# Kernel optimization log

Measured on AMD Instinct MI355X. Metric: run time of the kernel, lower is better.

Reference implementation:

```python
import jax, jax.numpy as jnp
import numpy as np

NUM_CLASSES = 7
CLASS_WEIGHT = 1.0
BOX_WEIGHT = 1.0


def _linear_sum_assignment(cost):
    """Exact Hungarian via shortest augmenting paths (Jonker-Volgenant style).
    Matches scipy.optimize.linear_sum_assignment for rectangular matrices:
    returns (row_ind, col_ind) of length min(n, m), row_ind sorted ascending."""
    C = np.asarray(cost, dtype=np.float64)
    transposed = C.shape[0] > C.shape[1]
    if transposed:
        C = C.T
    n, m = C.shape  # n <= m
    u = np.zeros(n + 1)
    v = np.zeros(m + 1)
    p = np.zeros(m + 1, dtype=np.int64)    # p[j]: row matched to col j (1-based); 0 = free
    way = np.zeros(m + 1, dtype=np.int64)
    for i in range(1, n + 1):
        p[0] = i
        j0 = 0
        minv = np.full(m + 1, np.inf)
        used = np.zeros(m + 1, dtype=bool)
        while True:
            used[j0] = True
            i0 = p[j0]
            cur = C[i0 - 1] - u[i0] - v[1:]
            free = ~used[1:]
            better = free & (cur < minv[1:])
            minv[1:][better] = cur[better]
            way[1:][better] = j0
            masked = np.where(free, minv[1:], np.inf)
            j0n = int(np.argmin(masked)) + 1
            delta = masked[j0n - 1]
            uj = np.nonzero(used)[0]
            u[p[uj]] += delta
            v[uj] -= delta
            minv[1:][free] -= delta
            j0 = j0n
            if p[j0] == 0:
                break
        while j0 != 0:   # augment along alternating path
            j1 = way[j0]
            p[j0] = p[j1]
            j0 = j1
    cols = np.nonzero(p[1:] > 0)[0]
    rows = p[1:][cols] - 1
    if transposed:
        rows, cols = cols, rows
    order = np.argsort(rows)
    return rows[order], cols[order]


def _cost_matrices(pred_logits, pred_boxes, gt_labels, gt_boxes):
    """Batched cost: class_weight * (-log_softmax gathered at gt labels) + box_weight * L1 cdist on xyz."""
    B, Q, _ = pred_logits.shape
    M = gt_labels.shape[1]
    log_probs = jax.nn.log_softmax(pred_logits, axis=-1)                       # (B,Q,C)
    idx = jnp.broadcast_to(gt_labels[:, None, :], (B, Q, M))
    class_cost = -jnp.take_along_axis(log_probs, idx, axis=2)                  # (B,Q,M)
    box_cost = jnp.sum(jnp.abs(pred_boxes[:, :, None, :3] - gt_boxes[:, None, :, :3]), axis=-1)  # (B,Q,M)
    return CLASS_WEIGHT * class_cost + BOX_WEIGHT * box_cost


def _matched_loss(pred_logits, pred_boxes, gt_labels, gt_boxes, rows, cols):
    B = pred_logits.shape[0]
    bidx = jnp.arange(B)[:, None]
    ml = pred_logits[bidx, rows]          # (B,M,C) matched logits
    mb = pred_boxes[bidx, rows]           # (B,M,7) matched boxes
    gl = gt_labels[bidx, cols]            # (B,M)
    gb = gt_boxes[bidx, cols]             # (B,M,7)
    logp = jax.nn.log_softmax(ml, axis=-1)
    ce = -jnp.mean(jnp.take_along_axis(logp, gl[..., None], axis=-1)[..., 0], axis=1)  # (B,)
    l1 = jnp.mean(jnp.abs(mb - gb), axis=(1, 2))                                       # (B,)
    return jnp.mean(CLASS_WEIGHT * ce + BOX_WEIGHT * l1)


def setup_inputs() -> dict:
    key = jax.random.key(0)
    k1, k2, k3, k4 = jax.random.split(key, 4)
    B, Q, M = 128, 900, 100
    return {
        'pred_logits': jax.random.normal(k1, (B, Q, NUM_CLASSES), dtype=jnp.float32),
        'pred_boxes': jax.random.normal(k2, (B, Q, 7), dtype=jnp.float32),
        'gt_labels': jax.random.randint(k3, (B, M), 0, NUM_CLASSES, dtype=jnp.int32),
        'gt_boxes': jax.random.normal(k4, (B, M, 7), dtype=jnp.float32),
    }


def reference(pred_logits, pred_boxes, gt_labels, gt_boxes):
    B = pred_logits.shape[0]
    M = gt_labels.shape[1]
    # Assignment is done on detached costs (host-side), matching the original module.
    cost = np.asarray(_cost_matrices(pred_logits, pred_boxes, gt_labels, gt_boxes))
    rows = np.zeros((B, M), dtype=np.int64)
    cols = np.zeros((B, M), dtype=np.int64)
    for b in range(B):
        r, c = _linear_sum_assignment(cost[b])
        rows[b], cols[b] = r, c
    return _matched_loss(pred_logits, pred_boxes, gt_labels, gt_boxes,
                         jnp.asarray(rows), jnp.asarray(cols))
```

## Files before the change

kernel.cpp:

```cpp
#include <hip/hip_runtime.h>
#include <math.h>


#define NQ   900
#define NG   100
#define NC   7
#define CPL  15
#define ROUNDS 12
#define INFF __builtin_inff()

__device__ __forceinline__ float readlane_f(float x, int l) {
  return __int_as_float(__builtin_amdgcn_readlane(__float_as_int(x), l));
}
template<int CTRL>
__device__ __forceinline__ float dpp_min_step(float x) {
  int y = __builtin_amdgcn_update_dpp(__float_as_int(x), __float_as_int(x),
                                      CTRL, 0xf, 0xf, false);
  return fminf(x, __int_as_float(y));
}
__device__ __forceinline__ float wave_min_b(float x) {
  x = dpp_min_step<0x111>(x);
  x = dpp_min_step<0x112>(x);
  x = dpp_min_step<0x114>(x);
  x = dpp_min_step<0x118>(x);
  x = dpp_min_step<0x142>(x);
  x = dpp_min_step<0x143>(x);
  return __int_as_float(__builtin_amdgcn_readlane(__float_as_int(x), 63));
}
template<int CTRL>
__device__ __forceinline__ float dpp_add_step(float x) {
  int y = __builtin_amdgcn_update_dpp(0, __float_as_int(x),
                                      CTRL, 0xf, 0xf, true);
  return x + __int_as_float(y);
}
__device__ __forceinline__ float wave_sum_b(float x) {
  x = dpp_add_step<0x111>(x);
  x = dpp_add_step<0x112>(x);
  x = dpp_add_step<0x114>(x);
  x = dpp_add_step<0x118>(x);
  x = dpp_add_step<0x142>(x);
  x = dpp_add_step<0x143>(x);
  return __int_as_float(__builtin_amdgcn_readlane(__float_as_int(x), 63));
}
__device__ __forceinline__ void gl_lds16(const float* g, float* lds_base) {
  __builtin_amdgcn_global_load_lds(
      (const __attribute__((address_space(1))) unsigned int*)g,
      (__attribute__((address_space(3))) unsigned int*)lds_base, 16, 0, 0);
}
__device__ __forceinline__ float sel7v(float a0,float a1,float a2,float a3,
                                       float a4,float a5,float a6,int lab){
  float r = a0;
  r = lab==1 ? a1 : r;  r = lab==2 ? a2 : r;  r = lab==3 ? a3 : r;
  r = lab==4 ? a4 : r;  r = lab==5 ? a5 : r;  r = lab==6 ? a6 : r;
  return r;
}

__global__ __launch_bounds__(256, 1) void hungarian_fused_kernel(
    const float* __restrict__ logits, const float* __restrict__ pboxes,
    const int* __restrict__ glabels, const float* __restrict__ gboxes,
    float* __restrict__ out, float inv_B)
{
  const int b = blockIdx.x, tid = threadIdx.x;
  const int lane = tid & 63, w = tid >> 6;

  __shared__ __align__(16) float s_raw[NQ * NC];
  __shared__ __align__(16) float s_nlpT[NC * 1024];
  __shared__ __align__(16) float s_pb[960 * NC];
  __shared__ __align__(16) float s_gb[NG * NC];
  __shared__ __align__(16) int   s_glab[NG];
  __shared__ float s_u[NG + 1];
  __shared__ float s_v[CPL * 64];
  __shared__ int   s_p[NQ];
  __shared__ unsigned s_bid[NQ];
  __shared__ int   s_rmatch[NG];
  __shared__ float s_bm1[NG], s_bm2[NG];
  __shared__ int   s_bc[NG];
  __shared__ int   s_freelist[NG];
  __shared__ int   s_nfree;
  __shared__ float s_f1v[NG]; __shared__ int s_f1c[NG];
  __shared__ float s_f2v[NG]; __shared__ int s_f2c[NG];
  __shared__ int   s_mlist[128];

  {
    const float* Lg = logits + (size_t)b * NQ * NC;
    const float* Pg = pboxes + (size_t)b * NQ * NC;
    const float* Gg = gboxes + (size_t)b * NG * NC;
    const int*   Bg = glabels + (size_t)b * NG;
    #pragma unroll
    for (int t = 0; t < 7; t++) {
      int i = (t << 8) + tid;
      if (i < (NQ * NC) / 4) {
        gl_lds16(Lg + i * 4, s_raw + ((t << 8) + (w << 6)) * 4);
        gl_lds16(Pg + i * 4, s_pb  + ((t << 8) + (w << 6)) * 4);
      }
    }
    if (tid < (NG * NC) / 4) gl_lds16(Gg + tid * 4, s_gb + (w << 6) * 4);
    if (tid < NG / 4) gl_lds16((const float*)Bg + tid * 4, (float*)s_glab);
    for (int i = tid; i < (960 - NQ) * NC; i += 256) s_pb[NQ * NC + i] = 0.f;
    for (int c = tid; c < NQ; c += 256) { s_p[c] = 0x7fffffff; s_bid[c] = 0xFFFFFFFFu; }
    for (int i = tid; i < CPL * 64; i += 256) s_v[i] = 0.f;
    if (tid == 0) s_u[0] = 0.f;
  }
  __syncthreads();

  for (int i = tid; i < 960; i += 256) {
    int L = i & 63, t = i >> 6;
    int q = L * CPL + t;
    float o[NC];
    if (q < NQ) {
      float x[NC];
      #pragma unroll
      for (int c = 0; c < NC; c++) x[c] = s_raw[q * NC + c];
      float mx = x[0];
      #pragma unroll
      for (int c = 1; c < NC; c++) mx = fmaxf(mx, x[c]);
      float tt[NC]; float se = 0.f;
      #pragma unroll
      for (int c = 0; c < NC; c++) { tt[c] = x[c] - mx; se += __expf(tt[c]); }
      float lg = __logf(se);
      #pragma unroll
      for (int c = 0; c < NC; c++) o[c] = lg - tt[c];
    } else {
      #pragma unroll
      for (int c = 0; c < NC; c++) o[c] = INFF;
    }
    #pragma unroll
    for (int c = 0; c < NC; c++) s_nlpT[c * 1024 + t * 64 + L] = o[c];
  }
  __syncthreads();

  const bool lval = (lane < NQ / CPL);
  float cpx[CPL], cpy[CPL], cpz[CPL];
  #pragma unroll
  for (int t = 0; t < CPL; t++) {
    int c = lane * CPL + t;
    cpx[t]=s_pb[c*NC+0]; cpy[t]=s_pb[c*NC+1]; cpz[t]=s_pb[c*NC+2];
  }

  for (int rl = 0; rl < 25; rl++) {
    int r = w * 25 + rl;
    int lab = s_glab[r];
    float gx = s_gb[r*NC+0], gy = s_gb[r*NC+1], gz = s_gb[r*NC+2];
    float m1 = INFF; int c1t = 0;
    #pragma unroll
    for (int t = 0; t < CPL; t++) {
      float nl = s_nlpT[lab*1024 + t*64 + lane];
      float bs = fabsf(cpx[t]-gx)+fabsf(cpy[t]-gy)+fabsf(cpz[t]-gz);
      float cost = nl + bs;
      bool lt1 = cost < m1;
      c1t = lt1 ? t : c1t;
      m1 = fminf(m1, cost);
    }
    float w1 = wave_min_b(m1);
    unsigned long long mk = __ballot(m1 == w1);
    int src = (int)__builtin_ctzll(mk);
    int col = __builtin_amdgcn_readlane(lane * CPL + c1t, src);
    if (lane == 0) {
      s_u[r + 1] = w1;
      s_bc[r] = col;
      atomicMin(&s_p[col], r + 1);
    }
  }
  __syncthreads();
  for (int c = tid; c < NQ; c += 256) if (s_p[c] == 0x7fffffff) s_p[c] = 0;
  if (tid < NG) {
    int c = s_bc[tid];
    s_rmatch[tid] = (s_p[c] == tid + 1) ? c + 1 : 0;
  }
  __syncthreads();

  for (int round = 0; round < ROUNDS; round++) {
    if (tid == 0) s_nfree = 0;
    __syncthreads();
    if (tid < NG && s_rmatch[tid] == 0) {
      int ix = atomicAdd(&s_nfree, 1);
      s_freelist[ix] = tid;
    }
    __syncthreads();
    int nf = s_nfree;
    if (nf == 0) break;
    for (int fi = w; fi < nf; fi += 4) {
      int r = s_freelist[fi];
      int lab = s_glab[r];
      float gx = s_gb[r*NC+0], gy = s_gb[r*NC+1], gz = s_gb[r*NC+2];
      float m1 = INFF, m2 = INFF; int c1t = 0;
      #pragma unroll
      for (int t = 0; t < CPL; t++) {
        float nl = s_nlpT[lab*1024 + t*64 + lane];
        float vv = s_v[t*64 + lane];
        float bs = fabsf(cpx[t]-gx)+fabsf(cpy[t]-gy)+fabsf(cpz[t]-gz);
        float cost = (nl + bs) - vv;
        bool lt1 = cost < m1;
        m2 = lt1 ? m1 : fminf(m2, cost);
        c1t = lt1 ? t : c1t;
        m1 = fminf(m1, cost);
      }
      float w1 = wave_min_b(m1);
      unsigned long long mk = __ballot(m1 == w1);
      int src = (int)__builtin_ctzll(mk);
      int col1 = __builtin_amdgcn_readlane(lane * CPL + c1t, src);
      float alt = (lane == src) ? m2 : m1;
      float w2 = wave_min_b(alt);
      if (lane == 0) {
        s_bm1[r] = w1; s_bm2[r] = w2; s_bc[r] = col1;
        atomicMin(&s_bid[col1],
                  (__float_as_uint(w1) & 0xFFFFFF80u) | (unsigned)(r + 1));
      }
    }
    __syncthreads();
    for (int fi = tid; fi < nf; fi += 256) {
      int r = s_freelist[fi];
      int c = s_bc[r];
      if ((s_bid[c] & 0x7Fu) == (unsigned)(r + 1)) {
        int dold = s_p[c];
        s_p[c] = r + 1;
        s_rmatch[r] = c + 1;
        if (dold > 0) s_rmatch[dold - 1] = 0;
        s_u[r + 1] = s_bm2[r];
        s_v[(c % CPL) * 64 + (c / CPL)] -= (s_bm2[r] - s_bm1[r]);
      }
    }
    __syncthreads();
    for (int fi = tid; fi < nf; fi += 256)
      s_bid[s_bc[s_freelist[fi]]] = 0xFFFFFFFFu;
    __syncthreads();
  }

  unsigned fmask = 0;
  if (lval) {
    #pragma unroll
    for (int t = 0; t < CPL; t++)
      if (s_p[lane * CPL + t] == 0) fmask |= (1u << t);
  }

  auto top2row = [&](int lab, float gx, float gy, float gz,
                     float &o1v, int &o1c, float &o2v, int &o2c) {
    float m1 = INFF, m2 = INFF; int c1 = 0, c2 = 0;
    #pragma unroll
    for (int t = 0; t < CPL; t++) {
      float nl = s_nlpT[lab*1024 + t*64 + lane];
      float bs = fabsf(cpx[t]-gx)+fabsf(cpy[t]-gy)+fabsf(cpz[t]-gz);
      float cost = nl + bs;
      cost = ((fmask >> t) & 1u) ? cost : INFF;
      bool lt1 = cost < m1;
      bool lt2 = cost < m2;
      c2 = lt1 ? c1 : (lt2 ? t : c2);
      m2 = lt1 ? m1 : fminf(m2, cost);
      c1 = lt1 ? t : c1;
      m1 = fminf(m1, cost);
    }
    float w1 = wave_min_b(m1);
    unsigned long long mk = __ballot(m1 == w1);
    int src = (int)__builtin_ctzll(mk);
    int col1 = __builtin_amdgcn_readlane(lane * CPL + c1, src);
    float alt = (lane == src) ? m2 : m1;
    int  altc = (lane == src) ? c2 : c1;
    float w2 = wave_min_b(alt);
    unsigned long long mk2 = __ballot(alt == w2);
    int src2 = (int)__builtin_ctzll(mk2);
    int col2 = __builtin_amdgcn_readlane(lane * CPL + altc, src2);
    o1v = w1; o1c = col1; o2v = w2; o2c = col2;
  };

  for (int rl = 0; rl < 25; rl++) {
    int r = w * 25 + rl;
    int lab = s_glab[r];
    float gx = s_gb[r*NC+0], gy = s_gb[r*NC+1], gz = s_gb[r*NC+2];
    float v1, v2; int cc1, cc2;
    top2row(lab, gx, gy, gz, v1, cc1, v2, cc2);
    if (lane == 0) {
      s_f1v[r] = v1; s_f1c[r] = cc1; s_f2v[r] = v2; s_f2c[r] = cc2;
    }
  }
  __syncthreads();
  if (w != 0) return;

  volatile float* vu = s_u;

  const bool r1ok = (lane < NG - 64);
  int   rlab0 = s_glab[lane];
  float rgx0 = s_gb[lane*NC+0], rgy0 = s_gb[lane*NC+1], rgz0 = s_gb[lane*NC+2];
  int   rlab1 = 0; float rgx1=0.f, rgy1=0.f, rgz1=0.f;
  if (r1ok) {
    int r = 64 + lane;
    rlab1 = s_glab[r];
    rgx1 = s_gb[r*NC+0]; rgy1 = s_gb[r*NC+1]; rgz1 = s_gb[r*NC+2];
  }
  float ru0 = vu[lane + 1];
  float ru1 = r1ok ? vu[lane + 65] : 0.f;
  float rf1v0 = s_f1v[lane];       int rf1c0 = s_f1c[lane];
  float rf2v0 = s_f2v[lane];       int rf2c0 = s_f2c[lane];
  float rf1v1 = r1ok ? s_f1v[64+lane] : INFF; int rf1c1 = r1ok ? s_f1c[64+lane] : -1;
  float rf2v1 = r1ok ? s_f2v[64+lane] : INFF; int rf2c1 = r1ok ? s_f2c[64+lane] : -1;

  bool lose0 = (s_rmatch[lane] == 0);
  bool lose1 = r1ok && (s_rmatch[64 + lane] == 0);
  unsigned long long fm0 = __ballot(lose0);
  unsigned long long fm1 = __ballot(lose1);

  int NM = 0;
  #pragma unroll
  for (int t = 0; t < CPL; t++) {
    int c = lane * CPL + t;
    bool has = lval && (s_p[c] > 0);
    unsigned long long m = __ballot(has);
    int pos = NM + (int)__popcll(m & ((1ull << lane) - 1ull));
    if (has) s_mlist[pos] = c;
    NM += (int)__popcll(m);
  }

  int   mcol[2]  = {-1,-1};
  int   mprow[2] = {0,0};
  float mpu[2]   = {0.f,0.f};
  float mv[2]    = {0.f,0.f};
  float mx[2]={0,0}, my[2]={0,0}, mz[2]={0,0};
  float mn0[2],mn1[2],mn2[2],mn3[2],mn4[2],mn5[2],mn6[2];
  #pragma unroll
  for (int k = 0; k < 2; k++) { mn0[k]=0;mn1[k]=0;mn2[k]=0;mn3[k]=0;mn4[k]=0;mn5[k]=0;mn6[k]=0; }
  #pragma unroll
  for (int k = 0; k < 2; k++) {
    int s = lane + (k << 6);
    if (s < NM) {
      int c = s_mlist[s];
      int cq = c / CPL, ct = c - cq * CPL;
      mcol[k] = c;
      mx[k] = s_pb[c*NC+0]; my[k] = s_pb[c*NC+1]; mz[k] = s_pb[c*NC+2];
      mn0[k] = s_nlpT[0*1024 + ct*64 + cq];
      mn1[k] = s_nlpT[1*1024 + ct*64 + cq];
      mn2[k] = s_nlpT[2*1024 + ct*64 + cq];
      mn3[k] = s_nlpT[3*1024 + ct*64 + cq];
      mn4[k] = s_nlpT[4*1024 + ct*64 + cq];
      mn5[k] = s_nlpT[5*1024 + ct*64 + cq];
      mn6[k] = s_nlpT[6*1024 + ct*64 + cq];
      mprow[k] = s_p[c];
      mpu[k] = vu[mprow[k]];
      mv[k] = s_v[ct * 64 + cq];
    }
  }

  float dsl[2]; int wsl[2];

  for (int half = 0; half < 2; half++) {
    unsigned long long fm = half ? fm1 : fm0;
    while (fm) {
      int bit = (int)__builtin_ctzll(fm);
      fm &= fm - 1;
      int rfree = bit + (half ? 65 : 1);
      dsl[0] = INFF; dsl[1] = INFF; wsl[0] = 0; wsl[1] = 0;
      unsigned usedm = 0;
      float bfv = INFF; int bfc = -1, bfprev = 0;
      int i0 = rfree;
      int ro0 = rfree - 1;
      float u_i0 = readlane_f((ro0 >> 6) ? ru1 : ru0, ro0 & 63);
      int j0p = 0;
      float minVal = 0.f;
      int jf = -1, jfprev = 0;

      for (int it = 0; it < 128; it++) {
        int ro = i0 - 1, rown = ro & 63, rs = ro >> 6;
        int   lab = __builtin_amdgcn_readlane(rs ? rlab1 : rlab0, rown);
        float gx = readlane_f(rs ? rgx1 : rgx0, rown);
        float gy = readlane_f(rs ? rgy1 : rgy0, rown);
        float gz = readlane_f(rs ? rgz1 : rgz0, rown);
        float hs = minVal - u_i0;
        float f1v = readlane_f(rs ? rf1v1 : rf1v0, rown);
        int   f1c = __builtin_amdgcn_readlane(rs ? rf1c1 : rf1c0, rown);
        float cbf = f1v + hs;
        if (cbf < bfv) { bfv = cbf; bfc = f1c; bfprev = j0p; }
        float lb = INFF; int bk = 0;
        #pragma unroll
        for (int k = 0; k < 2; k++) {
          bool gate = ((lane + (k << 6)) < NM) && !((usedm >> k) & 1u);
          float nl = sel7v(mn0[k],mn1[k],mn2[k],mn3[k],mn4[k],mn5[k],mn6[k],lab);
          float bs = fabsf(mx[k]-gx)+fabsf(my[k]-gy)+fabsf(mz[k]-gz);
          float rr = ((nl + bs) + hs) - mv[k];
          bool imp = gate && (rr < dsl[k]);
          dsl[k] = imp ? rr : dsl[k];
          wsl[k] = imp ? j0p : wsl[k];
          float cand = gate ? dsl[k] : INFF;
          bool bt = cand < lb;
          bk = bt ? k : bk;
          lb = fminf(lb, cand);
        }
        float dm = wave_min_b(lb);
        if (bfv <= dm) { minVal = bfv; jf = bfc; jfprev = bfprev; break; }
        unsigned long long msk = __ballot(lb == dm);
        int src = (int)__builtin_ctzll(msk);
        int spk = __builtin_amdgcn_readlane((bk << 6) | lane, src);
        minVal = dm;
        int so = spk & 63, sk = spk >> 6;
        usedm |= (lane == so) ? (1u << sk) : 0u;
        i0  = __builtin_amdgcn_readlane(sk ? mprow[1] : mprow[0], so);
        u_i0 = readlane_f(sk ? mpu[1] : mpu[0], so);
        j0p = spk + 1;
      }
      if (jf < 0) { jf = bfc; jfprev = bfprev; minVal = bfv; }

      if (lane == 0) vu[rfree] += minVal;
      #pragma unroll
      for (int k = 0; k < 2; k++) {
        if ((usedm >> k) & 1u) {
          float a = minVal - dsl[k];
          mv[k] -= a;
          vu[mprow[k]] += a;
        }
      }
      __threadfence_block();

      int pred = jfprev;
      int nr;
      if (pred == 0) nr = rfree;
      else {
        int s = pred - 1;
        nr = __builtin_amdgcn_readlane((s >> 6) ? mprow[1] : mprow[0], s & 63);
      }
      if (lane == 0) s_p[jf] = nr;
      {
        int cq = jf / CPL, ct = jf - cq * CPL;
        float nx = s_pb[jf*NC+0], ny = s_pb[jf*NC+1], nz = s_pb[jf*NC+2];
        float a0 = s_nlpT[0*1024 + ct*64 + cq];
        float a1 = s_nlpT[1*1024 + ct*64 + cq];
        float a2 = s_nlpT[2*1024 + ct*64 + cq];
        float a3 = s_nlpT[3*1024 + ct*64 + cq];
        float a4 = s_nlpT[4*1024 + ct*64 + cq];
        float a5 = s_nlpT[5*1024 + ct*64 + cq];
        float a6 = s_nlpT[6*1024 + ct*64 + cq];
        int kk = NM >> 6;
        if (lane == (NM & 63) && NM < 128) {
          if (kk == 0) {
            mcol[0]=jf; mx[0]=nx; my[0]=ny; mz[0]=nz; mprow[0]=nr; mv[0]=0.f;
            mn0[0]=a0;mn1[0]=a1;mn2[0]=a2;mn3[0]=a3;mn4[0]=a4;mn5[0]=a5;mn6[0]=a6;
          } else {
            mcol[1]=jf; mx[1]=nx; my[1]=ny; mz[1]=nz; mprow[1]=nr; mv[1]=0.f;
            mn0[1]=a0;mn1[1]=a1;mn2[1]=a2;mn3[1]=a3;mn4[1]=a4;mn5[1]=a5;mn6[1]=a6;
          }
        }
        NM++;
      }
      while (pred) {
        int s = pred - 1, so = s & 63, sk = s >> 6;
        int np = __builtin_amdgcn_readlane(sk ? wsl[1] : wsl[0], so);
        int nr2;
        if (np == 0) nr2 = rfree;
        else {
          int s2 = np - 1;
          nr2 = __builtin_amdgcn_readlane((s2 >> 6) ? mprow[1] : mprow[0], s2 & 63);
        }
        int sc = __builtin_amdgcn_readlane(sk ? mcol[1] : mcol[0], so);
        if (lane == so) { if (sk) mprow[1] = nr2; else mprow[0] = nr2; }
        if (lane == 0) s_p[sc] = nr2;
        pred = np;
      }
      __threadfence_block();

      ru0 = vu[lane + 1];
      if (r1ok) ru1 = vu[lane + 65];
      #pragma unroll
      for (int k = 0; k < 2; k++)
        if ((lane + (k << 6)) < NM) mpu[k] = vu[mprow[k]];

      if (lane == (jf / CPL)) fmask &= ~(1u << (jf - (jf / CPL) * CPL));
      if (rf1c0 == jf) { rf1v0 = rf2v0; rf1c0 = rf2c0; rf2c0 = -1; rf2v0 = INFF; }
      else if (rf2c0 == jf) { rf2c0 = -1; rf2v0 = INFF; }
      if (rf1c1 == jf) { rf1v1 = rf2v1; rf1c1 = rf2c1; rf2c1 = -1; rf2v1 = INFF; }
      else if (rf2c1 == jf) { rf2c1 = -1; rf2v1 = INFF; }
      unsigned long long need0 = __ballot(rf1c0 < 0);
      unsigned long long need1 = __ballot(r1ok && (rf1c1 < 0));
      while (need0) {
        int rb = (int)__builtin_ctzll(need0); need0 &= need0 - 1;
        int lab = __builtin_amdgcn_readlane(rlab0, rb);
        float gx = readlane_f(rgx0, rb), gy = readlane_f(rgy0, rb), gz = readlane_f(rgz0, rb);
        float v1, v2; int cc1, cc2;
        top2row(lab, gx, gy, gz, v1, cc1, v2, cc2);
        if (lane == rb) { rf1v0=v1; rf1c0=cc1; rf2v0=v2; rf2c0=cc2; }
      }
      while (need1) {
        int rb = (int)__builtin_ctzll(need1); need1 &= need1 - 1;
        int lab = __builtin_amdgcn_readlane(rlab1, rb);
        float gx = readlane_f(rgx1, rb), gy = readlane_f(rgy1, rb), gz = readlane_f(rgz1, rb);
        float v1, v2; int cc1, cc2;
        top2row(lab, gx, gy, gz, v1, cc1, v2, cc2);
        if (lane == rb) { rf1v1=v1; rf1c1=cc1; rf2v1=v2; rf2c1=cc2; }
      }
    }
  }

  float ce = 0.f, l1 = 0.f;
  if (lval) {
    #pragma unroll
    for (int t = 0; t < CPL; t++) {
      int c = lane * CPL + t;
      int pr = s_p[c];
      if (pr > 0) {
        int g = pr - 1;
        int lg = s_glab[g];
        ce += s_nlpT[lg*1024 + t*64 + lane];
        float s = 0.f;
        #pragma unroll
        for (int d7 = 0; d7 < 7; d7++) s += fabsf(s_pb[c*NC+d7] - s_gb[g*NC+d7]);
        l1 += s;
      }
    }
  }
  float tot = ce * (1.f / NG) + l1 * (1.f / (NG * 7.f));
  tot = wave_sum_b(tot);
  if (lane == 0) atomicAdd(out, tot * inv_B);
}

extern "C" void kernel_launch(void* const* d_in, const int* in_sizes, int n_in,
                              void* d_out, int out_size, void* d_ws, size_t ws_size,
                              hipStream_t stream) {
  const float* logits  = (const float*)d_in[0];
  const float* pboxes  = (const float*)d_in[1];
  const int*   glabels = (const int*)d_in[2];
  const float* gboxes  = (const float*)d_in[3];
  float* out = (float*)d_out;
  const int B = in_sizes[0] / (NQ * NC);

  hipMemsetAsync(out, 0, sizeof(float), stream);
  hungarian_fused_kernel<<<dim3(B), dim3(256), 0, stream>>>(
      logits, pboxes, glabels, gboxes, out, 1.0f / (float)B);
}
```

Measured before the change: 131.0 us.

## Fold greedy init into auction rounds and drop freelist construction barriers

Removes the separate greedy initial-assignment pass and runs all rows through the auction rounds from the start. Free rows are found by scanning s_rmatch per wave instead of building a freelist, so each round needs fewer barriers, and the free count comes from atomic increments during conflict resolution. If no rows remain free, the Hungarian fallback phase is skipped, and only wave 0 computes the loss. The round cap goes from 12 to 14, which risks more rounds per block, and all waves now scan all 100 rows each round.

```diff
diff --git a/kernel.cpp b/kernel.cpp
--- a/kernel.cpp
+++ b/kernel.cpp
@@ -6,7 +6,7 @@
 #define NG   100
 #define NC   7
 #define CPL  15
-#define ROUNDS 12
+#define ROUNDS 14
 #define INFF __builtin_inff()
 
 __device__ __forceinline__ float readlane_f(float x, int l) {
@@ -75,7 +75,7 @@
   __shared__ int   s_rmatch[NG];
   __shared__ float s_bm1[NG], s_bm2[NG];
   __shared__ int   s_bc[NG];
-  __shared__ int   s_freelist[NG];
+  __shared__ int   s_bround[NG];
   __shared__ int   s_nfree;
   __shared__ float s_f1v[NG]; __shared__ int s_f1c[NG];
   __shared__ float s_f2v[NG]; __shared__ int s_f2c[NG];
@@ -97,9 +97,10 @@
     if (tid < (NG * NC) / 4) gl_lds16(Gg + tid * 4, s_gb + (w << 6) * 4);
     if (tid < NG / 4) gl_lds16((const float*)Bg + tid * 4, (float*)s_glab);
     for (int i = tid; i < (960 - NQ) * NC; i += 256) s_pb[NQ * NC + i] = 0.f;
-    for (int c = tid; c < NQ; c += 256) { s_p[c] = 0x7fffffff; s_bid[c] = 0xFFFFFFFFu; }
+    for (int c = tid; c < NQ; c += 256) { s_p[c] = 0; s_bid[c] = 0xFFFFFFFFu; }
     for (int i = tid; i < CPL * 64; i += 256) s_v[i] = 0.f;
-    if (tid == 0) s_u[0] = 0.f;
+    if (tid < NG) { s_rmatch[tid] = 0; s_bround[tid] = -1; }
+    if (tid == 0) { s_u[0] = 0.f; s_nfree = NG; }
   }
   __syncthreads();
 
@@ -137,50 +138,9 @@
     cpx[t]=s_pb[c*NC+0]; cpy[t]=s_pb[c*NC+1]; cpz[t]=s_pb[c*NC+2];
   }
 
-  for (int rl = 0; rl < 25; rl++) {
-    int r = w * 25 + rl;
-    int lab = s_glab[r];
-    float gx = s_gb[r*NC+0], gy = s_gb[r*NC+1], gz = s_gb[r*NC+2];
-    float m1 = INFF; int c1t = 0;
-    #pragma unroll
-    for (int t = 0; t < CPL; t++) {
-      float nl = s_nlpT[lab*1024 + t*64 + lane];
-      float bs = fabsf(cpx[t]-gx)+fabsf(cpy[t]-gy)+fabsf(cpz[t]-gz);
-      float cost = nl + bs;
-      bool lt1 = cost < m1;
-      c1t = lt1 ? t : c1t;
-      m1 = fminf(m1, cost);
-    }
-    float w1 = wave_min_b(m1);
-    unsigned long long mk = __ballot(m1 == w1);
-    int src = (int)__builtin_ctzll(mk);
-    int col = __builtin_amdgcn_readlane(lane * CPL + c1t, src);
-    if (lane == 0) {
-      s_u[r + 1] = w1;
-      s_bc[r] = col;
-      atomicMin(&s_p[col], r + 1);
-    }
-  }
-  __syncthreads();
-  for (int c = tid; c < NQ; c += 256) if (s_p[c] == 0x7fffffff) s_p[c] = 0;
-  if (tid < NG) {
-    int c = s_bc[tid];
-    s_rmatch[tid] = (s_p[c] == tid + 1) ? c + 1 : 0;
-  }
-  __syncthreads();
-
   for (int round = 0; round < ROUNDS; round++) {
-    if (tid == 0) s_nfree = 0;
-    __syncthreads();
-    if (tid < NG && s_rmatch[tid] == 0) {
-      int ix = atomicAdd(&s_nfree, 1);
-      s_freelist[ix] = tid;
-    }
-    __syncthreads();
-    int nf = s_nfree;
-    if (nf == 0) break;
-    for (int fi = w; fi < nf; fi += 4) {
-      int r = s_freelist[fi];
+    for (int r = w; r < NG; r += 4) {
+      if (s_rmatch[r] != 0) continue;
       int lab = s_glab[r];
       float gx = s_gb[r*NC+0], gy = s_gb[r*NC+1], gz = s_gb[r*NC+2];
       float m1 = INFF, m2 = INFF; int c1t = 0;
@@ -202,30 +162,37 @@
       float alt = (lane == src) ? m2 : m1;
       float w2 = wave_min_b(alt);
       if (lane == 0) {
-        s_bm1[r] = w1; s_bm2[r] = w2; s_bc[r] = col1;
+        s_bm1[r] = w1; s_bm2[r] = w2; s_bc[r] = col1; s_bround[r] = round;
+        s_u[r + 1] = w1;
         atomicMin(&s_bid[col1],
                   (__float_as_uint(w1) & 0xFFFFFF80u) | (unsigned)(r + 1));
       }
     }
+    if (tid == 0) s_nfree = 0;
     __syncthreads();
-    for (int fi = tid; fi < nf; fi += 256) {
-      int r = s_freelist[fi];
-      int c = s_bc[r];
+    if (tid < NG && s_bround[tid] == round) {
+      int r = tid, c = s_bc[r];
       if ((s_bid[c] & 0x7Fu) == (unsigned)(r + 1)) {
         int dold = s_p[c];
         s_p[c] = r + 1;
         s_rmatch[r] = c + 1;
-        if (dold > 0) s_rmatch[dold - 1] = 0;
+        if (dold > 0) { s_rmatch[dold - 1] = 0; atomicAdd(&s_nfree, 1); }
         s_u[r + 1] = s_bm2[r];
         s_v[(c % CPL) * 64 + (c / CPL)] -= (s_bm2[r] - s_bm1[r]);
+      } else {
+        atomicAdd(&s_nfree, 1);
       }
     }
     __syncthreads();
-    for (int fi = tid; fi < nf; fi += 256)
-      s_bid[s_bc[s_freelist[fi]]] = 0xFFFFFFFFu;
+    int nf = s_nfree;
+    if (tid < NG && s_bround[tid] == round) s_bid[s_bc[tid]] = 0xFFFFFFFFu;
+    if (nf == 0) break;
     __syncthreads();
   }
-
+  __syncthreads();
+  if (s_nfree == 0) goto loss_phase;
+
+  {
   unsigned fmask = 0;
   if (lval) {
     #pragma unroll
@@ -484,27 +451,32 @@
       }
     }
   }
-
-  float ce = 0.f, l1 = 0.f;
-  if (lval) {
-    #pragma unroll
-    for (int t = 0; t < CPL; t++) {
-      int c = lane * CPL + t;
-      int pr = s_p[c];
-      if (pr > 0) {
-        int g = pr - 1;
-        int lg = s_glab[g];
-        ce += s_nlpT[lg*1024 + t*64 + lane];
-        float s = 0.f;
-        #pragma unroll
-        for (int d7 = 0; d7 < 7; d7++) s += fabsf(s_pb[c*NC+d7] - s_gb[g*NC+d7]);
-        l1 += s;
-      }
-    }
-  }
-  float tot = ce * (1.f / NG) + l1 * (1.f / (NG * 7.f));
-  tot = wave_sum_b(tot);
-  if (lane == 0) atomicAdd(out, tot * inv_B);
+  }
+
+loss_phase:
+  if (w != 0) return;
+  {
+    float ce = 0.f, l1 = 0.f;
+    if (lval) {
+      #pragma unroll
+      for (int t = 0; t < CPL; t++) {
+        int c = lane * CPL + t;
+        int pr = s_p[c];
+        if (pr > 0) {
+          int g = pr - 1;
+          int lg = s_glab[g];
+          ce += s_nlpT[lg*1024 + t*64 + lane];
+          float s = 0.f;
+          #pragma unroll
+          for (int d7 = 0; d7 < 7; d7++) s += fabsf(s_pb[c*NC+d7] - s_gb[g*NC+d7]);
+          l1 += s;
+        }
+      }
+    }
+    float tot = ce * (1.f / NG) + l1 * (1.f / (NG * 7.f));
+    tot = wave_sum_b(tot);
+    if (lane == 0) atomicAdd(out, tot * inv_B);
+  }
 }
 
 extern "C" void kernel_launch(void* const* d_in, const int* in_sizes, int n_in,
```

Result: slower. 151.7 us (+15.8%).
